# Kernel tuning notes

Hardware: AMD Instinct MI355X
Metric: run time of the kernel (lower is better)

The kernel has to match this reference:

```python
import jax, jax.numpy as jnp
import numpy as np

N = 50000      # nodes
E = 1600000    # edges
F_IN = 128
H = 128
C = 10
G = 512        # graphs in batch


def setup_inputs() -> dict:
    key = jax.random.key(0)
    ks = jax.random.split(key, 16)
    x = jax.random.normal(ks[0], (N, F_IN), dtype=jnp.float32)
    edge_index = jax.random.randint(ks[1], (2, E), 0, N, dtype=jnp.int64)
    edge_weight = jax.random.uniform(ks[2], (E,), dtype=jnp.float32)
    batch = jnp.sort(jax.random.randint(ks[3], (N,), 0, G, dtype=jnp.int64))
    s = 0.05
    params = {
        'W0': jax.random.normal(ks[4], (H, F_IN), dtype=jnp.float32) * s,
        'b0': jnp.zeros((H,), dtype=jnp.float32),
        'W1': jax.random.normal(ks[5], (H, H), dtype=jnp.float32) * s,
        'b1': jnp.zeros((H,), dtype=jnp.float32),
        'W2': jax.random.normal(ks[6], (H, H), dtype=jnp.float32) * s,
        'b2': jnp.zeros((H,), dtype=jnp.float32),
        'W3': jax.random.normal(ks[7], (H, H), dtype=jnp.float32) * s,
        'b3': jnp.zeros((H,), dtype=jnp.float32),
        'fc1_w': jax.random.normal(ks[8], (H, H), dtype=jnp.float32) * s,
        'fc1_b': jnp.zeros((H,), dtype=jnp.float32),
        'fc2_w': jax.random.normal(ks[9], (C, H), dtype=jnp.float32) * s,
        'fc2_b': jnp.zeros((C,), dtype=jnp.float32),
    }
    return dict(x=x, edge_index=edge_index, edge_weight=edge_weight, batch=batch, **params)


def _gcn_norm(edge_index, edge_weight):
    # PyG gcn_norm with add_self_loops=True (fill_value=1.0)
    loop = jnp.arange(N, dtype=edge_index.dtype)
    row = jnp.concatenate([edge_index[0], loop])  # source
    col = jnp.concatenate([edge_index[1], loop])  # target
    w = jnp.concatenate([edge_weight, jnp.ones((N,), dtype=edge_weight.dtype)])
    deg = jax.ops.segment_sum(w, col, num_segments=N)
    dinv = jnp.where(deg > 0, jax.lax.rsqrt(deg), 0.0)
    norm = dinv[row] * w * dinv[col]  # [E+N]
    return row, col, norm


def _gcn_conv(h, W, b, row, col, norm):
    h = h @ W.T                                   # [N, out]
    msg = h[row] * norm[:, None]                  # gather + scale [E+N, out]
    out = jax.ops.segment_sum(msg, col, num_segments=N)
    return out + b


def reference(x, edge_index, edge_weight, batch,
              W0, b0, W1, b1, W2, b2, W3, b3,
              fc1_w, fc1_b, fc2_w, fc2_b):
    row, col, norm = _gcn_norm(edge_index, edge_weight)
    h = x
    for W, b in ((W0, b0), (W1, b1), (W2, b2), (W3, b3)):
        h = _gcn_conv(h, W, b, row, col, norm)
        h = jax.nn.elu(h)  # dropout p=0 / eval -> identity
    # global_mean_pool over batch ids
    sums = jax.ops.segment_sum(h, batch, num_segments=G)            # [G, H]
    cnt = jax.ops.segment_sum(jnp.ones((N,), h.dtype), batch, num_segments=G)
    pooled = sums / jnp.maximum(cnt, 1.0)[:, None]
    z = jax.nn.elu(pooled @ fc1_w.T + fc1_b)
    z = z @ fc2_w.T + fc2_b
    return jax.nn.log_softmax(z, axis=1)
```

## Files before the change

kernel.cpp:

```cpp
#include <hip/hip_runtime.h>
#include <math.h>

#define N_NODES 50000
#define N_EDGES 1600000
#define HDIM 128
#define NGRAPH 512
#define NCLS 10

#define NSLICE 256
#define EDGES_PER_SLICE (N_EDGES / NSLICE)
#define BSH 7
#define NBUCK 391

typedef __attribute__((ext_vector_type(8))) short short8v;
typedef __attribute__((ext_vector_type(4))) float float4v;
typedef __attribute__((ext_vector_type(2))) float float2v;

__device__ inline float blo(unsigned int v) { return __uint_as_float(v << 16); }
__device__ inline float bhi(unsigned int v) { return __uint_as_float(v & 0xffff0000u); }
__device__ inline float b2f(unsigned short u) { return __uint_as_float(((unsigned)u) << 16); }
__device__ inline unsigned short f2b(float f) {
  unsigned int u = __float_as_uint(f);
  unsigned int r = u + 0x7fffu + ((u >> 16) & 1u);
  return (unsigned short)(r >> 16);
}
__device__ inline unsigned char f2fp8(float f) {
  return (unsigned char)(__builtin_amdgcn_cvt_pk_fp8_f32(f, 0.f, 0, false) & 0xFF);
}
__device__ inline float2v fp8x2lo(unsigned int u) {
  return __builtin_amdgcn_cvt_pk_f32_fp8(u, false);
}
__device__ inline float2v fp8x2hi(unsigned int u) {
  return __builtin_amdgcn_cvt_pk_f32_fp8(u, true);
}

__global__ __launch_bounds__(256) void cast4_k(const float* __restrict__ in, unsigned short* __restrict__ out, int n4) {
  int i = blockIdx.x * 256 + threadIdx.x;
  if (i < n4) {
    float4 v = ((const float4*)in)[i];
    ushort4 o;
    o.x = f2b(v.x); o.y = f2b(v.y); o.z = f2b(v.z); o.w = f2b(v.w);
    ((ushort4*)out)[i] = o;
  }
}

__global__ __launch_bounds__(256) void castw_k(const float* __restrict__ w0, const float* __restrict__ w1,
                                               const float* __restrict__ w2, const float* __restrict__ w3,
                                               unsigned short* __restrict__ o0, unsigned short* __restrict__ o1,
                                               unsigned short* __restrict__ o2, unsigned short* __restrict__ o3) {
  int i = blockIdx.x * 256 + threadIdx.x;
  int l = i >> 12, j = i & 4095;
  const float* in = (l == 0) ? w0 : (l == 1) ? w1 : (l == 2) ? w2 : w3;
  unsigned short* out = (l == 0) ? o0 : (l == 1) ? o1 : (l == 2) ? o2 : o3;
  float4 v = ((const float4*)in)[j];
  ushort4 o;
  o.x = f2b(v.x); o.y = f2b(v.y); o.z = f2b(v.z); o.w = f2b(v.w);
  ((ushort4*)out)[j] = o;
}

__global__ __launch_bounds__(256) void countA_k(const int* __restrict__ ei, int* __restrict__ partialB) {
  __shared__ int cnt[NBUCK];
  int s = blockIdx.x, t = threadIdx.x;
  for (int i = t; i < NBUCK; i += 256) cnt[i] = 0;
  __syncthreads();
  int base = s * EDGES_PER_SLICE;
  for (int i = t; i < EDGES_PER_SLICE; i += 256) {
    int c = ei[N_EDGES + base + i];
    atomicAdd(&cnt[c >> BSH], 1);
  }
  __syncthreads();
  for (int i = t; i < NBUCK; i += 256) partialB[s * NBUCK + i] = cnt[i];
}

__global__ __launch_bounds__(256) void prefixA1_k(int* __restrict__ partialB, int* __restrict__ boff) {
  int b = blockIdx.x * 256 + threadIdx.x;
  if (b >= NBUCK) return;
  int acc = 0;
  for (int s = 0; s < NSLICE; ++s) {
    int v = partialB[s * NBUCK + b];
    partialB[s * NBUCK + b] = acc;
    acc += v;
  }
  boff[b] = acc;
}

__global__ __launch_bounds__(512) void prefixA2_k(int* __restrict__ boff) {
  __shared__ int sd[512];
  int t = threadIdx.x;
  int my = (t < NBUCK) ? boff[t] : 0;
  sd[t] = my;
  __syncthreads();
  for (int d = 1; d < 512; d <<= 1) {
    int v = (t >= d) ? sd[t - d] : 0;
    __syncthreads();
    sd[t] += v;
    __syncthreads();
  }
  if (t < NBUCK) boff[t] = sd[t] - my;
  if (t == 511) boff[NBUCK] = sd[511];
}

__global__ __launch_bounds__(256) void bucketA_k(const int* __restrict__ ei, const float* __restrict__ ew,
                                                 const int* __restrict__ partialB, const int* __restrict__ boff,
                                                 unsigned long long* __restrict__ bucketed) {
  __shared__ int rnk[NBUCK];
  __shared__ int sbase[NBUCK];
  int s = blockIdx.x, t = threadIdx.x;
  for (int i = t; i < NBUCK; i += 256) { rnk[i] = 0; sbase[i] = boff[i] + partialB[s * NBUCK + i]; }
  __syncthreads();
  int base = s * EDGES_PER_SLICE;
  for (int i = t; i < EDGES_PER_SLICE; i += 256) {
    int c = ei[N_EDGES + base + i];
    int r = ei[base + i];
    float w = ew[base + i];
    int bk = c >> BSH;
    int rank = atomicAdd(&rnk[bk], 1);
    unsigned long long v = ((unsigned long long)__float_as_uint(w) << 32)
                         | ((unsigned long long)(unsigned)r << BSH)
                         | (unsigned long long)(c & 127);
    bucketed[(size_t)sbase[bk] + rank] = v;
  }
}

__global__ __launch_bounds__(256) void csrB_k(const unsigned long long* __restrict__ bucketed,
                                              const int* __restrict__ boff,
                                              int* __restrict__ off, float* __restrict__ dinv,
                                              unsigned int* __restrict__ cpack) {
  __shared__ int cnt[128];
  __shared__ float wsum[128];
  __shared__ int sc[128];
  __shared__ int cnt2[128];
  int b = blockIdx.x, t = threadIdx.x;
  if (t < 128) { cnt[t] = 0; cnt2[t] = 0; wsum[t] = 1.0f; }
  __syncthreads();
  int s = boff[b], e = boff[b + 1];
  for (int i = s + t; i < e; i += 256) {
    unsigned long long v = bucketed[i];
    atomicAdd(&cnt[(int)(v & 127)], 1);
    atomicAdd(&wsum[(int)(v & 127)], __uint_as_float((unsigned)(v >> 32)));
  }
  __syncthreads();
  if (t < 128) sc[t] = cnt[t];
  __syncthreads();
  for (int d = 1; d < 128; d <<= 1) {
    int v = (t < 128 && t >= d) ? sc[t - d] : 0;
    __syncthreads();
    if (t < 128) sc[t] += v;
    __syncthreads();
  }
  int node = b * 128 + t;
  if (t < 128 && node < N_NODES) {
    off[node] = s + sc[t] - cnt[t];
    dinv[node] = rsqrtf(wsum[t]);
  }
  __syncthreads();
  for (int i = s + t; i < e; i += 256) {
    unsigned long long v = bucketed[i];
    int cl = (int)(v & 127);
    int r = (int)((v >> BSH) & 0xFFFF);
    float w = __uint_as_float((unsigned)(v >> 32));
    int rank = atomicAdd(&cnt2[cl], 1);
    int pos = s + sc[cl] - cnt[cl] + rank;
    cpack[pos] = ((unsigned int)f2b(w) << 16) | (unsigned int)r;
  }
  if (b == 0 && t == 0) off[N_NODES] = N_EDGES;
}

__global__ __launch_bounds__(256) void gemm_mfma_k(const unsigned short* __restrict__ A,
                                                   const unsigned short* __restrict__ W16,
                                                   const float* __restrict__ dinv,
                                                   unsigned char* __restrict__ Out8) {
  __shared__ unsigned short Wl[128 * 128];
  int t = threadIdx.x;
  for (int idx = t; idx < 2048; idx += 256) {
    int n = idx >> 4, G = idx & 15;
    short8v v = *(const short8v*)(W16 + n * 128 + G * 8);
    int Gs = G ^ (n & 15);
    *(short8v*)(&Wl[n * 128 + Gs * 8]) = v;
  }
  __syncthreads();

  int wave = t >> 6, lane = t & 63;
  int l15 = lane & 15, l4 = lane >> 4;
  int rbase = blockIdx.x * 128 + wave * 32;

  float4v acc[2][8];
#pragma unroll
  for (int m = 0; m < 2; ++m)
#pragma unroll
    for (int f = 0; f < 8; ++f) acc[m][f] = (float4v){0.f, 0.f, 0.f, 0.f};

  int r0 = rbase + l15;        if (r0 >= N_NODES) r0 = N_NODES - 1;
  int r1 = rbase + 16 + l15;   if (r1 >= N_NODES) r1 = N_NODES - 1;

#pragma unroll
  for (int s = 0; s < 4; ++s) {
    int kk = s * 32 + l4 * 8;
    short8v a0 = *(const short8v*)(A + (size_t)r0 * 128 + kk);
    short8v a1 = *(const short8v*)(A + (size_t)r1 * 128 + kk);
#pragma unroll
    for (int f = 0; f < 8; ++f) {
      int n = f * 16 + l15;
      int G = s * 4 + l4;
      int Gs = G ^ (n & 15);
      short8v bfr = *(const short8v*)(&Wl[n * 128 + Gs * 8]);
      acc[0][f] = __builtin_amdgcn_mfma_f32_16x16x32_bf16(a0, bfr, acc[0][f], 0, 0, 0);
      acc[1][f] = __builtin_amdgcn_mfma_f32_16x16x32_bf16(a1, bfr, acc[1][f], 0, 0, 0);
    }
  }

#pragma unroll
  for (int m = 0; m < 2; ++m) {
    int rb = rbase + m * 16 + l4 * 4;
#pragma unroll
    for (int r = 0; r < 4; ++r) {
      int row = rb + r;
      if (row < N_NODES) {
        float ds = dinv[row];
        unsigned char* orow = Out8 + (size_t)row * 128 + l15;
#pragma unroll
        for (int f = 0; f < 8; ++f) orow[f * 16] = f2fp8(acc[m][f][r] * ds);
      }
    }
  }
}

__global__ __launch_bounds__(256) void aggregate_k(const unsigned char* __restrict__ h8,
                                                   const float* __restrict__ dinv,
                                                   const int* __restrict__ off,
                                                   const unsigned int* __restrict__ cpack,
                                                   const float* __restrict__ bias,
                                                   unsigned short* __restrict__ hout) {
  int c = blockIdx.x * 16 + (threadIdx.x >> 4);
  if (c >= N_NODES) return;
  int fl = threadIdx.x & 15;
  const uint2* h8q = (const uint2*)h8;
  uint2 sv = h8q[((size_t)c << 4) + fl];
  float2v s0 = fp8x2lo(sv.x), s1 = fp8x2hi(sv.x), s2 = fp8x2lo(sv.y), s3 = fp8x2hi(sv.y);
  float a0 = s0.x, a1 = s0.y, a2 = s1.x, a3 = s1.y;
  float a4 = s2.x, a5 = s2.y, a6 = s3.x, a7 = s3.y;
  int s = off[c], e = off[c + 1];
  int k = s;
  for (; k + 8 <= e; k += 8) {
    unsigned int p0 = cpack[k],   p1 = cpack[k+1], p2 = cpack[k+2], p3 = cpack[k+3];
    unsigned int p4 = cpack[k+4], p5 = cpack[k+5], p6 = cpack[k+6], p7 = cpack[k+7];
    uint2 g0 = h8q[((size_t)(p0 & 0xFFFF) << 4) + fl];
    uint2 g1 = h8q[((size_t)(p1 & 0xFFFF) << 4) + fl];
    uint2 g2 = h8q[((size_t)(p2 & 0xFFFF) << 4) + fl];
    uint2 g3 = h8q[((size_t)(p3 & 0xFFFF) << 4) + fl];
    uint2 g4 = h8q[((size_t)(p4 & 0xFFFF) << 4) + fl];
    uint2 g5 = h8q[((size_t)(p5 & 0xFFFF) << 4) + fl];
    uint2 g6 = h8q[((size_t)(p6 & 0xFFFF) << 4) + fl];
    uint2 g7 = h8q[((size_t)(p7 & 0xFFFF) << 4) + fl];
    float w0 = bhi(p0), w1 = bhi(p1), w2 = bhi(p2), w3 = bhi(p3);
    float w4 = bhi(p4), w5 = bhi(p5), w6 = bhi(p6), w7 = bhi(p7);
#define AGG_EDGE(G, W) { \
    float2v q0 = fp8x2lo(G.x), q1 = fp8x2hi(G.x), q2 = fp8x2lo(G.y), q3 = fp8x2hi(G.y); \
    a0 += W * q0.x; a1 += W * q0.y; a2 += W * q1.x; a3 += W * q1.y; \
    a4 += W * q2.x; a5 += W * q2.y; a6 += W * q3.x; a7 += W * q3.y; }
    AGG_EDGE(g0, w0) AGG_EDGE(g1, w1) AGG_EDGE(g2, w2) AGG_EDGE(g3, w3)
    AGG_EDGE(g4, w4) AGG_EDGE(g5, w5) AGG_EDGE(g6, w6) AGG_EDGE(g7, w7)
  }
  for (; k < e; ++k) {
    unsigned int p = cpack[k];
    uint2 g = h8q[((size_t)(p & 0xFFFF) << 4) + fl];
    float w = bhi(p);
    AGG_EDGE(g, w)
  }
#undef AGG_EDGE
  float dc = dinv[c];
  int col = fl * 8;
  float4 b0 = *(const float4*)(bias + col);
  float4 b1 = *(const float4*)(bias + col + 4);
  a0 = dc * a0 + b0.x;  a1 = dc * a1 + b0.y;  a2 = dc * a2 + b0.z;  a3 = dc * a3 + b0.w;
  a4 = dc * a4 + b1.x;  a5 = dc * a5 + b1.y;  a6 = dc * a6 + b1.z;  a7 = dc * a7 + b1.w;
  a0 = a0 > 0.f ? a0 : expm1f(a0);
  a1 = a1 > 0.f ? a1 : expm1f(a1);
  a2 = a2 > 0.f ? a2 : expm1f(a2);
  a3 = a3 > 0.f ? a3 : expm1f(a3);
  a4 = a4 > 0.f ? a4 : expm1f(a4);
  a5 = a5 > 0.f ? a5 : expm1f(a5);
  a6 = a6 > 0.f ? a6 : expm1f(a6);
  a7 = a7 > 0.f ? a7 : expm1f(a7);
  short8v o;
  o[0] = (short)f2b(a0); o[1] = (short)f2b(a1); o[2] = (short)f2b(a2); o[3] = (short)f2b(a3);
  o[4] = (short)f2b(a4); o[5] = (short)f2b(a5); o[6] = (short)f2b(a6); o[7] = (short)f2b(a7);
  *(short8v*)(hout + (size_t)c * 128 + col) = o;
}

__global__ __launch_bounds__(512) void poolhead_k(const unsigned short* __restrict__ h,
                                                  const int* __restrict__ batch,
                                                  const float* __restrict__ fc1w, const float* __restrict__ fc1b,
                                                  const float* __restrict__ fc2w, const float* __restrict__ fc2b,
                                                  float* __restrict__ out) {
  __shared__ float part[8][HDIM];
  __shared__ float ps[HDIM];
  __shared__ float z1[HDIM];
  __shared__ float z2[NCLS];
  int g = blockIdx.x, t = threadIdx.x;
  int fl = t & 63;
  int grp = t >> 6;
  int lo = 0, hi = N_NODES;
  while (lo < hi) { int mid = (lo + hi) >> 1; if (batch[mid] < g) lo = mid + 1; else hi = mid; }
  int gs = lo;
  hi = N_NODES;
  while (lo < hi) { int mid = (lo + hi) >> 1; if (batch[mid] < g + 1) lo = mid + 1; else hi = mid; }
  int ge = lo;
  const unsigned int* hw = (const unsigned int*)h;
  float a0 = 0.f, a1 = 0.f;
  for (int n = gs + grp; n < ge; n += 8) {
    unsigned int v = hw[((size_t)n << 6) + fl];
    a0 += blo(v); a1 += bhi(v);
  }
  part[grp][fl * 2] = a0;
  part[grp][fl * 2 + 1] = a1;
  __syncthreads();
  if (t < HDIM) {
    float s = 0.f;
#pragma unroll
    for (int q = 0; q < 8; ++q) s += part[q][t];
    ps[t] = s / (float)max(ge - gs, 1);
  }
  __syncthreads();
  if (t < HDIM) {
    float acc = fc1b[t];
    for (int i = 0; i < HDIM; ++i) acc += ps[i] * fc1w[t * HDIM + i];
    z1[t] = (acc > 0.f) ? acc : expm1f(acc);
  }
  __syncthreads();
  if (t < NCLS) {
    float a2 = fc2b[t];
    for (int i = 0; i < HDIM; ++i) a2 += z1[i] * fc2w[t * HDIM + i];
    z2[t] = a2;
  }
  __syncthreads();
  if (t == 0) {
    float m = -1e30f;
    for (int i = 0; i < NCLS; ++i) m = fmaxf(m, z2[i]);
    float s2 = 0.f;
    for (int i = 0; i < NCLS; ++i) s2 += expf(z2[i] - m);
    float l = logf(s2);
    for (int i = 0; i < NCLS; ++i) out[g * NCLS + i] = z2[i] - m - l;
  }
}

static inline size_t align256(size_t x) { return (x + 255) & ~(size_t)255; }

extern "C" void kernel_launch(void* const* d_in, const int* in_sizes, int n_in,
                              void* d_out, int out_size, void* d_ws, size_t ws_size,
                              hipStream_t stream) {
  const float* x     = (const float*)d_in[0];
  const int*   ei    = (const int*)d_in[1];
  const float* ew    = (const float*)d_in[2];
  const int*   batch = (const int*)d_in[3];
  const float* Wl[4] = { (const float*)d_in[4], (const float*)d_in[6], (const float*)d_in[8], (const float*)d_in[10] };
  const float* bl[4] = { (const float*)d_in[5], (const float*)d_in[7], (const float*)d_in[9], (const float*)d_in[11] };
  const float* fc1w = (const float*)d_in[12];
  const float* fc1b = (const float*)d_in[13];
  const float* fc2w = (const float*)d_in[14];
  const float* fc2b = (const float*)d_in[15];
  float* out = (float*)d_out;

  char* ws = (char*)d_ws;
  size_t o = 0;
  unsigned short* x16 = (unsigned short*)(ws + o); o = align256(o + (size_t)N_NODES * HDIM * 2);
  unsigned short* h16 = (unsigned short*)(ws + o); o = align256(o + (size_t)N_NODES * HDIM * 2);
  unsigned char* h8 = (unsigned char*)(ws + o);
  unsigned long long* bucketed = (unsigned long long*)(ws + o);
  o = align256(o + (size_t)N_EDGES * 8);
  unsigned short* w16[4];
  for (int l = 0; l < 4; ++l) { w16[l] = (unsigned short*)(ws + o); o = align256(o + (size_t)HDIM * HDIM * 2); }
  unsigned int* cpack = (unsigned int*)(ws + o); o = align256(o + (size_t)N_EDGES * 4);
  int*   partialB = (int*)(ws + o);   o = align256(o + (size_t)NSLICE * NBUCK * 4);
  int*   boff     = (int*)(ws + o);   o = align256(o + (size_t)(NBUCK + 1) * 4);
  float* dinv  = (float*)(ws + o); o = align256(o + (size_t)N_NODES * 4);
  int*   off   = (int*)  (ws + o); o = align256(o + (size_t)(N_NODES + 1) * 4);

  cast4_k<<<(N_NODES * HDIM / 4 + 255) / 256, 256, 0, stream>>>(x, x16, N_NODES * HDIM / 4);
  castw_k<<<64, 256, 0, stream>>>(Wl[0], Wl[1], Wl[2], Wl[3], w16[0], w16[1], w16[2], w16[3]);

  countA_k<<<NSLICE, 256, 0, stream>>>(ei, partialB);
  prefixA1_k<<<(NBUCK + 255) / 256, 256, 0, stream>>>(partialB, boff);
  prefixA2_k<<<1, 512, 0, stream>>>(boff);
  bucketA_k<<<NSLICE, 256, 0, stream>>>(ei, ew, partialB, boff, bucketed);
  csrB_k<<<NBUCK, 256, 0, stream>>>(bucketed, boff, off, dinv, cpack);

  const unsigned short* hin = x16;
  for (int l = 0; l < 4; ++l) {
    gemm_mfma_k<<<(N_NODES + 127) / 128, 256, 0, stream>>>(hin, w16[l], dinv, h8);
    aggregate_k<<<(N_NODES + 15) / 16, 256, 0, stream>>>(h8, dinv, off, cpack, bl[l], h16);
    hin = h16;
  }

  poolhead_k<<<NGRAPH, 512, 0, stream>>>(h16, batch, fc1w, fc1b, fc2w, fc2b, out);
}
```

Measured before the change: 259.2 us.

## Degree-sort nodes for aggregation, double GEMM rows per block, add nontemporal hints

Adds a counting sort of nodes by in-degree (count, scan, scatter kernels) and has the aggregation kernel process nodes in that permuted order. Nodes with similar edge counts then share a wavefront, which reduces divergence and load imbalance between the 16-lane groups. The GEMM kernel now covers 256 rows per block in two passes, so the shared-memory weight load is amortised over more rows. Streaming loads and stores for A, cpack and hout become nontemporal to reduce cache pollution. The cost is three extra small kernel launches and the loss of contiguous node order, which may hurt locality on the output writes.

```diff
diff --git a/kernel.cpp b/kernel.cpp
--- a/kernel.cpp
+++ b/kernel.cpp
@@ -11,6 +11,9 @@
 #define EDGES_PER_SLICE (N_EDGES / NSLICE)
 #define BSH 7
 #define NBUCK 391
+
+#define DPART 64
+#define NODES_PER_DBLK ((N_NODES + DPART - 1) / DPART)
 
 typedef __attribute__((ext_vector_type(8))) short short8v;
 typedef __attribute__((ext_vector_type(4))) float float4v;
@@ -166,6 +169,56 @@
   if (b == 0 && t == 0) off[N_NODES] = N_EDGES;
 }
 
+__global__ __launch_bounds__(256) void degcnt_k(const int* __restrict__ off, int* __restrict__ partialD) {
+  __shared__ int cnt[256];
+  int s = blockIdx.x, t = threadIdx.x;
+  cnt[t] = 0;
+  __syncthreads();
+  int lo = s * NODES_PER_DBLK, hi = min(lo + NODES_PER_DBLK, N_NODES);
+  for (int n = lo + t; n < hi; n += 256) {
+    int d = min(off[n + 1] - off[n], 255);
+    atomicAdd(&cnt[d], 1);
+  }
+  __syncthreads();
+  partialD[s * 256 + t] = cnt[t];
+}
+
+__global__ __launch_bounds__(256) void degscan_k(int* __restrict__ partialD) {
+  __shared__ int tot[256];
+  int t = threadIdx.x;
+  int acc = 0;
+  for (int s = 0; s < DPART; ++s) {
+    int v = partialD[s * 256 + t];
+    partialD[s * 256 + t] = acc;
+    acc += v;
+  }
+  int my = acc;
+  tot[t] = my;
+  __syncthreads();
+  for (int d = 1; d < 256; d <<= 1) {
+    int v = (t >= d) ? tot[t - d] : 0;
+    __syncthreads();
+    tot[t] += v;
+    __syncthreads();
+  }
+  int base = tot[t] - my;
+  for (int s = 0; s < DPART; ++s) partialD[s * 256 + t] += base;
+}
+
+__global__ __launch_bounds__(256) void degscat_k(const int* __restrict__ off, const int* __restrict__ partialD,
+                                                 int* __restrict__ perm) {
+  __shared__ int rnk[256];
+  int s = blockIdx.x, t = threadIdx.x;
+  rnk[t] = partialD[s * 256 + t];
+  __syncthreads();
+  int lo = s * NODES_PER_DBLK, hi = min(lo + NODES_PER_DBLK, N_NODES);
+  for (int n = lo + t; n < hi; n += 256) {
+    int d = min(off[n + 1] - off[n], 255);
+    int pos = atomicAdd(&rnk[d], 1);
+    perm[pos] = n;
+  }
+}
+
 __global__ __launch_bounds__(256) void gemm_mfma_k(const unsigned short* __restrict__ A,
                                                    const unsigned short* __restrict__ W16,
                                                    const float* __restrict__ dinv,
@@ -182,44 +235,48 @@
 
   int wave = t >> 6, lane = t & 63;
   int l15 = lane & 15, l4 = lane >> 4;
-  int rbase = blockIdx.x * 128 + wave * 32;
-
-  float4v acc[2][8];
-#pragma unroll
-  for (int m = 0; m < 2; ++m)
-#pragma unroll
-    for (int f = 0; f < 8; ++f) acc[m][f] = (float4v){0.f, 0.f, 0.f, 0.f};
-
-  int r0 = rbase + l15;        if (r0 >= N_NODES) r0 = N_NODES - 1;
-  int r1 = rbase + 16 + l15;   if (r1 >= N_NODES) r1 = N_NODES - 1;
-
-#pragma unroll
-  for (int s = 0; s < 4; ++s) {
-    int kk = s * 32 + l4 * 8;
-    short8v a0 = *(const short8v*)(A + (size_t)r0 * 128 + kk);
-    short8v a1 = *(const short8v*)(A + (size_t)r1 * 128 + kk);
-#pragma unroll
-    for (int f = 0; f < 8; ++f) {
-      int n = f * 16 + l15;
-      int G = s * 4 + l4;
-      int Gs = G ^ (n & 15);
-      short8v bfr = *(const short8v*)(&Wl[n * 128 + Gs * 8]);
-      acc[0][f] = __builtin_amdgcn_mfma_f32_16x16x32_bf16(a0, bfr, acc[0][f], 0, 0, 0);
-      acc[1][f] = __builtin_amdgcn_mfma_f32_16x16x32_bf16(a1, bfr, acc[1][f], 0, 0, 0);
+
+#pragma unroll
+  for (int j = 0; j < 2; ++j) {
+    int rbase = blockIdx.x * 256 + j * 128 + wave * 32;
+
+    float4v acc[2][8];
+#pragma unroll
+    for (int m = 0; m < 2; ++m)
+#pragma unroll
+      for (int f = 0; f < 8; ++f) acc[m][f] = (float4v){0.f, 0.f, 0.f, 0.f};
+
+    int r0 = rbase + l15;        if (r0 >= N_NODES) r0 = N_NODES - 1;
+    int r1 = rbase + 16 + l15;   if (r1 >= N_NODES) r1 = N_NODES - 1;
+
+#pragma unroll
+    for (int s = 0; s < 4; ++s) {
+      int kk = s * 32 + l4 * 8;
+      short8v a0 = __builtin_nontemporal_load((const short8v*)(A + (size_t)r0 * 128 + kk));
+      short8v a1 = __builtin_nontemporal_load((const short8v*)(A + (size_t)r1 * 128 + kk));
+#pragma unroll
+      for (int f = 0; f < 8; ++f) {
+        int n = f * 16 + l15;
+        int G = s * 4 + l4;
+        int Gs = G ^ (n & 15);
+        short8v bfr = *(const short8v*)(&Wl[n * 128 + Gs * 8]);
+        acc[0][f] = __builtin_amdgcn_mfma_f32_16x16x32_bf16(a0, bfr, acc[0][f], 0, 0, 0);
+        acc[1][f] = __builtin_amdgcn_mfma_f32_16x16x32_bf16(a1, bfr, acc[1][f], 0, 0, 0);
+      }
     }
-  }
-
-#pragma unroll
-  for (int m = 0; m < 2; ++m) {
-    int rb = rbase + m * 16 + l4 * 4;
-#pragma unroll
-    for (int r = 0; r < 4; ++r) {
-      int row = rb + r;
-      if (row < N_NODES) {
-        float ds = dinv[row];
-        unsigned char* orow = Out8 + (size_t)row * 128 + l15;
-#pragma unroll
-        for (int f = 0; f < 8; ++f) orow[f * 16] = f2fp8(acc[m][f][r] * ds);
+
+#pragma unroll
+    for (int m = 0; m < 2; ++m) {
+      int rb = rbase + m * 16 + l4 * 4;
+#pragma unroll
+      for (int r = 0; r < 4; ++r) {
+        int row = rb + r;
+        if (row < N_NODES) {
+          float ds = dinv[row];
+          unsigned char* orow = Out8 + (size_t)row * 128 + l15;
+#pragma unroll
+          for (int f = 0; f < 8; ++f) orow[f * 16] = f2fp8(acc[m][f][r] * ds);
+        }
       }
     }
   }
@@ -229,10 +286,11 @@
                                                    const float* __restrict__ dinv,
                                                    const int* __restrict__ off,
                                                    const unsigned int* __restrict__ cpack,
+                                                   const int* __restrict__ perm,
                                                    const float* __restrict__ bias,
                                                    unsigned short* __restrict__ hout) {
-  int c = blockIdx.x * 16 + (threadIdx.x >> 4);
-  if (c >= N_NODES) return;
+  int gid = blockIdx.x * 16 + (threadIdx.x >> 4);
+  int c = perm[gid];
   int fl = threadIdx.x & 15;
   const uint2* h8q = (const uint2*)h8;
   uint2 sv = h8q[((size_t)c << 4) + fl];
@@ -242,8 +300,14 @@
   int s = off[c], e = off[c + 1];
   int k = s;
   for (; k + 8 <= e; k += 8) {
-    unsigned int p0 = cpack[k],   p1 = cpack[k+1], p2 = cpack[k+2], p3 = cpack[k+3];
-    unsigned int p4 = cpack[k+4], p5 = cpack[k+5], p6 = cpack[k+6], p7 = cpack[k+7];
+    unsigned int p0 = __builtin_nontemporal_load(&cpack[k]);
+    unsigned int p1 = __builtin_nontemporal_load(&cpack[k + 1]);
+    unsigned int p2 = __builtin_nontemporal_load(&cpack[k + 2]);
+    unsigned int p3 = __builtin_nontemporal_load(&cpack[k + 3]);
+    unsigned int p4 = __builtin_nontemporal_load(&cpack[k + 4]);
+    unsigned int p5 = __builtin_nontemporal_load(&cpack[k + 5]);
+    unsigned int p6 = __builtin_nontemporal_load(&cpack[k + 6]);
+    unsigned int p7 = __builtin_nontemporal_load(&cpack[k + 7]);
     uint2 g0 = h8q[((size_t)(p0 & 0xFFFF) << 4) + fl];
     uint2 g1 = h8q[((size_t)(p1 & 0xFFFF) << 4) + fl];
     uint2 g2 = h8q[((size_t)(p2 & 0xFFFF) << 4) + fl];
@@ -262,7 +326,7 @@
     AGG_EDGE(g4, w4) AGG_EDGE(g5, w5) AGG_EDGE(g6, w6) AGG_EDGE(g7, w7)
   }
   for (; k < e; ++k) {
-    unsigned int p = cpack[k];
+    unsigned int p = __builtin_nontemporal_load(&cpack[k]);
     uint2 g = h8q[((size_t)(p & 0xFFFF) << 4) + fl];
     float w = bhi(p);
     AGG_EDGE(g, w)
@@ -285,7 +349,7 @@
   short8v o;
   o[0] = (short)f2b(a0); o[1] = (short)f2b(a1); o[2] = (short)f2b(a2); o[3] = (short)f2b(a3);
   o[4] = (short)f2b(a4); o[5] = (short)f2b(a5); o[6] = (short)f2b(a6); o[7] = (short)f2b(a7);
-  *(short8v*)(hout + (size_t)c * 128 + col) = o;
+  __builtin_nontemporal_store(o, (short8v*)(hout + (size_t)c * 128 + col));
 }
 
 __global__ __launch_bounds__(512) void poolhead_k(const unsigned short* __restrict__ h,
@@ -375,6 +439,8 @@
   int*   boff     = (int*)(ws + o);   o = align256(o + (size_t)(NBUCK + 1) * 4);
   float* dinv  = (float*)(ws + o); o = align256(o + (size_t)N_NODES * 4);
   int*   off   = (int*)  (ws + o); o = align256(o + (size_t)(N_NODES + 1) * 4);
+  int*   partialD = (int*)(ws + o); o = align256(o + (size_t)DPART * 256 * 4);
+  int*   perm     = (int*)(ws + o); o = align256(o + (size_t)N_NODES * 4);
 
   cast4_k<<<(N_NODES * HDIM / 4 + 255) / 256, 256, 0, stream>>>(x, x16, N_NODES * HDIM / 4);
   castw_k<<<64, 256, 0, stream>>>(Wl[0], Wl[1], Wl[2], Wl[3], w16[0], w16[1], w16[2], w16[3]);
@@ -385,10 +451,14 @@
   bucketA_k<<<NSLICE, 256, 0, stream>>>(ei, ew, partialB, boff, bucketed);
   csrB_k<<<NBUCK, 256, 0, stream>>>(bucketed, boff, off, dinv, cpack);
 
+  degcnt_k<<<DPART, 256, 0, stream>>>(off, partialD);
+  degscan_k<<<1, 256, 0, stream>>>(partialD);
+  degscat_k<<<DPART, 256, 0, stream>>>(off, partialD, perm);
+
   const unsigned short* hin = x16;
   for (int l = 0; l < 4; ++l) {
-    gemm_mfma_k<<<(N_NODES + 127) / 128, 256, 0, stream>>>(hin, w16[l], dinv, h8);
-    aggregate_k<<<(N_NODES + 15) / 16, 256, 0, stream>>>(h8, dinv, off, cpack, bl[l], h16);
+    gemm_mfma_k<<<(N_NODES + 255) / 256, 256, 0, stream>>>(hin, w16[l], dinv, h8);
+    aggregate_k<<<(N_NODES + 15) / 16, 256, 0, stream>>>(h8, dinv, off, cpack, perm, bl[l], h16);
     hin = h16;
   }
 
```

Measured after the change: 302.2 us. 1.17x slower.
